# Performance work log

Hardware: AMD Instinct MI355X
Metric: run time of the kernel (lower is better)

Reference implementation:

```python
import jax, jax.numpy as jnp
import numpy as np

N_HEADS = 4
D_K = 64

def setup_inputs() -> dict:
    key = jax.random.key(0)
    k1, k2, k3 = jax.random.split(key, 3)
    B, C, H, W = 16, 256, 32, 32
    x = jax.random.normal(k1, (B, C, H, W), dtype=jnp.float32)
    # Linear(C, 3*n_heads*d_k) stored as [in, out] for x @ W
    w_proj = jax.random.normal(k2, (C, 3 * N_HEADS * D_K), dtype=jnp.float32) * (1.0 / np.sqrt(C))
    b_proj = jnp.zeros((3 * N_HEADS * D_K,), dtype=jnp.float32)
    w_out = jax.random.normal(k3, (N_HEADS * D_K, C), dtype=jnp.float32) * (1.0 / np.sqrt(N_HEADS * D_K))
    b_out = jnp.zeros((C,), dtype=jnp.float32)
    return {"x": x, "w_proj": w_proj, "b_proj": b_proj, "w_out": w_out, "b_out": b_out}

def reference(x, w_proj, b_proj, w_out, b_out):
    B, C, H, W = x.shape
    S = H * W
    scale = D_K ** -0.5
    xs = x.reshape(B, C, S).transpose(0, 2, 1)            # [B, S, C]
    qkv = (xs @ w_proj + b_proj).reshape(B, S, N_HEADS, 3 * D_K)
    q, k, v = jnp.split(qkv, 3, axis=3)                    # each [B, S, H, dk]
    attn = jnp.einsum('bihd,bjhd->bijh', q, k) * scale     # [B, S, S, heads]
    attn = jax.nn.softmax(attn, axis=2)
    o = jnp.einsum('bijh,bjhd->bihd', attn, v)             # [B, S, heads, dk]
    o = o.reshape(B, S, N_HEADS * D_K)
    res = o @ w_out + b_out + xs                           # [B, S, C]
    return res.transpose(0, 2, 1).reshape(B, C, H, W)
```

## Files before the change

### kernel.cpp

```cpp
#include <hip/hip_runtime.h>
#include <math.h>

#define B_  16
#define C_  256
#define S_  1024
#define NH  4
#define DK  64
#define P3  768
#define ND  256

typedef unsigned short u16;
typedef unsigned int   u32;
typedef float  f32x4  __attribute__((ext_vector_type(4)));
typedef short  bf16x8 __attribute__((ext_vector_type(8)));

#define MFMA16(a, b, c) __builtin_amdgcn_mfma_f32_16x16x32_bf16(a, b, c, 0, 0, 0)

#define QSCALE 0.1803368801111137f

__device__ __forceinline__ u16 f2bf(float f) {
    union { float f; u32 u; } x; x.f = f;
    u32 r = x.u + 0x7fffu + ((x.u >> 16) & 1u);
    return (u16)(r >> 16);
}

__device__ __forceinline__ void stage16(const u16* g, u16* l) {
    __builtin_amdgcn_global_load_lds(
        (const __attribute__((address_space(1))) void*)g,
        (__attribute__((address_space(3))) void*)l, 16, 0, 0);
}

__global__ __launch_bounds__(256) void transpose_cvt(
    const float* __restrict__ src, u16* __restrict__ dst, int R, int Cc)
{
    __shared__ float T[64][65];
    const int tid = threadIdx.x;
    const int c0 = blockIdx.x * 64, r0 = blockIdx.y * 64, z = blockIdx.z;
    src += (size_t)z * R * Cc;
    dst += (size_t)z * R * Cc;

    const int l64 = tid & 63, rr0 = tid >> 6;
    #pragma unroll
    for (int t = 0; t < 16; ++t) {
        int rr = rr0 + t * 4;
        T[rr][l64] = src[(size_t)(r0 + rr) * Cc + c0 + l64];
    }
    __syncthreads();
    const int rp = tid & 31;
    const int cb = tid >> 5;
    #pragma unroll
    for (int t = 0; t < 8; ++t) {
        int c = cb + t * 8;
        u32 lo = f2bf(T[2 * rp][c]);
        u32 hi = f2bf(T[2 * rp + 1][c]);
        *(u32*)&dst[(size_t)(c0 + c) * R + r0 + 2 * rp] = lo | (hi << 16);
    }
}

__global__ __launch_bounds__(256) void transpose_w(
    const float* __restrict__ wp, u16* __restrict__ wpT,
    const float* __restrict__ wo, u16* __restrict__ woT)
{
    const int z = blockIdx.z;
    const int Cc = z ? 256 : 768;
    if ((int)blockIdx.x * 64 >= Cc) return;
    const float* src = z ? wo : wp;
    u16* dst = z ? woT : wpT;
    const int R = 256;

    __shared__ float T[64][65];
    const int tid = threadIdx.x;
    const int c0 = blockIdx.x * 64, r0 = blockIdx.y * 64;

    const int l64 = tid & 63, rr0 = tid >> 6;
    #pragma unroll
    for (int t = 0; t < 16; ++t) {
        int rr = rr0 + t * 4;
        T[rr][l64] = src[(size_t)(r0 + rr) * Cc + c0 + l64];
    }
    __syncthreads();
    const int rp = tid & 31;
    const int cb = tid >> 5;
    #pragma unroll
    for (int t = 0; t < 8; ++t) {
        int c = cb + t * 8;
        u32 lo = f2bf(T[2 * rp][c]);
        u32 hi = f2bf(T[2 * rp + 1][c]);
        *(u32*)&dst[(size_t)(c0 + c) * R + r0 + 2 * rp] = lo | (hi << 16);
    }
}

__global__ __launch_bounds__(256) void qkv_mfma(
    const u16* __restrict__ xt, const u16* __restrict__ wpT,
    const float* __restrict__ bp, u16* __restrict__ qo,
    u16* __restrict__ ko, u16* __restrict__ vo)
{
    __shared__ __align__(16) u16 SM[24576];
    u16* As = SM;
    u16* Bs = SM + 16384;

    const int tid = threadIdx.x;
    const int w = tid >> 6, lane = tid & 63;
    const int n_ = lane & 15, quad = lane >> 4;
    const int n0 = blockIdx.x * 64, s0 = blockIdx.y * 128, b = blockIdx.z;

    const u16* ar0 = xt + ((size_t)b * S_ + s0 + (2 * w + 0) * 16 + n_) * C_ + quad * 8;
    const u16* ar1 = xt + ((size_t)b * S_ + s0 + (2 * w + 1) * 16 + n_) * C_ + quad * 8;
    const u16* br  = wpT + (size_t)(n0 + w * 16 + n_) * C_ + quad * 8;

    f32x4 acc[2][4];
    #pragma unroll
    for (int am = 0; am < 2; ++am)
        #pragma unroll
        for (int nf = 0; nf < 4; ++nf)
            #pragma unroll
            for (int r = 0; r < 4; ++r) acc[am][nf][r] = 0.f;

    #pragma unroll
    for (int kb = 0; kb < 2; ++kb) {
        const int kcb = kb * 128;
        __syncthreads();
        #pragma unroll
        for (int kc = 0; kc < 4; ++kc) {
            stage16(ar0 + kcb + kc * 32, As + ((2 * w + 0) * 4 + kc) * 512);
            stage16(ar1 + kcb + kc * 32, As + ((2 * w + 1) * 4 + kc) * 512);
            stage16(br  + kcb + kc * 32, Bs + (w * 4 + kc) * 512);
        }
        __syncthreads();
        #pragma unroll
        for (int kc = 0; kc < 4; ++kc) {
            bf16x8 af0 = *(const bf16x8*)&As[((2 * w + 0) * 4 + kc) * 512 + lane * 8];
            bf16x8 af1 = *(const bf16x8*)&As[((2 * w + 1) * 4 + kc) * 512 + lane * 8];
            #pragma unroll
            for (int nf = 0; nf < 4; ++nf) {
                bf16x8 bf = *(const bf16x8*)&Bs[(nf * 4 + kc) * 512 + lane * 8];
                acc[0][nf] = MFMA16(af0, bf, acc[0][nf]);
                acc[1][nf] = MFMA16(af1, bf, acc[1][nf]);
            }
        }
    }

    const int hd = n0 / 192, rem = n0 % 192, which = rem / 64;
    const int bh = b * NH + hd;
    float bias[4];
    #pragma unroll
    for (int nf = 0; nf < 4; ++nf) bias[nf] = bp[n0 + nf * 16 + n_];
    const float sc = (which == 0) ? QSCALE : 1.f;

    __syncthreads();
    if (which < 2) {
        u16* Cs = SM;
        #pragma unroll
        for (int am = 0; am < 2; ++am) {
            int row0 = w * 32 + am * 16 + quad * 4;
            #pragma unroll
            for (int nf = 0; nf < 4; ++nf)
                #pragma unroll
                for (int r = 0; r < 4; ++r)
                    Cs[(row0 + r) * 72 + nf * 16 + n_] =
                        f2bf((acc[am][nf][r] + bias[nf]) * sc);
        }
        __syncthreads();
        u16* dst = (which == 0) ? qo : ko;
        #pragma unroll
        for (int t = 0; t < 4; ++t) {
            int ii = tid + t * 256;
            int row = ii >> 3, c8 = (ii & 7) * 8;
            *(bf16x8*)&dst[((size_t)bh * S_ + s0 + row) * DK + c8] =
                *(const bf16x8*)&Cs[row * 72 + c8];
        }
    } else {
        u16* Cs = SM;
        #pragma unroll
        for (int am = 0; am < 2; ++am) {
            int colb = w * 32 + am * 16 + quad * 4;
            #pragma unroll
            for (int nf = 0; nf < 4; ++nf)
                #pragma unroll
                for (int r = 0; r < 4; ++r)
                    Cs[(nf * 16 + n_) * 136 + colb + r] =
                        f2bf(acc[am][nf][r] + bias[nf]);
        }
        __syncthreads();
        #pragma unroll
        for (int t = 0; t < 4; ++t) {
            int ii = tid + t * 256;
            int row = ii >> 4, c8 = (ii & 15) * 8;
            *(bf16x8*)&vo[((size_t)bh * DK + row) * S_ + s0 + c8] =
                *(const bf16x8*)&Cs[row * 136 + c8];
        }
    }
}

__global__ __launch_bounds__(256) void attn_mfma(
    const u16* __restrict__ q, const u16* __restrict__ k,
    const u16* __restrict__ vt, u16* __restrict__ obf)
{
    __shared__ __align__(16) u16 SM[9216];
    u16* Ks = SM;
    u16* Vs = SM + 4096;

    const int tid = threadIdx.x;
    const int w = tid >> 6, lane = tid & 63;
    const int n_ = lane & 15, quad = lane >> 4;
    const int i0 = blockIdx.x * 128;
    const int hd = blockIdx.y, b = blockIdx.z;
    const int bh = b * NH + hd;

    bf16x8 qf[2][2];
    #pragma unroll
    for (int am = 0; am < 2; ++am) {
        const u16* qrow = q + ((size_t)bh * S_ + i0 + w * 32 + am * 16 + n_) * DK;
        qf[am][0] = *(const bf16x8*)&qrow[quad * 8];
        qf[am][1] = *(const bf16x8*)&qrow[32 + quad * 8];
    }

    const int kappa = 32 * (w & 1) + 8 * (n_ >> 2) + 4 * (w >> 1) + (n_ & 3);
    const u16* kbase = k  + ((size_t)bh * S_ + kappa) * DK + quad * 8;
    const u16* vbase = vt + ((size_t)bh * DK + w * 16 + n_) * S_ + quad * 8;

    float lsum[2] = {0.f, 0.f};
    f32x4 oacc[2][4];
    #pragma unroll
    for (int am = 0; am < 2; ++am)
        #pragma unroll
        for (int nd = 0; nd < 4; ++nd)
            #pragma unroll
            for (int r = 0; r < 4; ++r) oacc[am][nd][r] = 0.f;

    for (int jt = 0; jt < S_; jt += 64) {
        __syncthreads();
        stage16(kbase + (size_t)jt * DK,      Ks + w * 1024);
        stage16(kbase + (size_t)jt * DK + 32, Ks + w * 1024 + 512);
        stage16(vbase + jt,                   Vs + w * 1024);
        stage16(vbase + jt + 32,              Vs + w * 1024 + 512);
        __syncthreads();

        f32x4 sb[2][4];
        #pragma unroll
        for (int nb = 0; nb < 4; ++nb) {
            bf16x8 kf0 = *(const bf16x8*)&Ks[nb * 1024 + lane * 8];
            bf16x8 kf1 = *(const bf16x8*)&Ks[nb * 1024 + 512 + lane * 8];
            #pragma unroll
            for (int am = 0; am < 2; ++am) {
                f32x4 a; a[0] = a[1] = a[2] = a[3] = 0.f;
                a = MFMA16(kf0, qf[am][0], a);
                a = MFMA16(kf1, qf[am][1], a);
                sb[am][nb] = a;
            }
        }

        bf16x8 pa[2][2];
        #pragma unroll
        for (int am = 0; am < 2; ++am) {
            u32 tr[4][4];
            #pragma unroll
            for (int nb = 0; nb < 4; ++nb)
                #pragma unroll
                for (int r = 0; r < 4; ++r) {
                    float p = exp2f(sb[am][nb][r]);
                    u32 bits = __float_as_uint(p) & 0xffff0000u;
                    lsum[am] += __uint_as_float(bits);
                    tr[nb][r] = bits;
                }
            union { bf16x8 v; u32 u[4]; } p0, p1;
            p0.u[0] = (tr[0][0] >> 16) | tr[0][1];
            p0.u[1] = (tr[0][2] >> 16) | tr[0][3];
            p0.u[2] = (tr[2][0] >> 16) | tr[2][1];
            p0.u[3] = (tr[2][2] >> 16) | tr[2][3];
            p1.u[0] = (tr[1][0] >> 16) | tr[1][1];
            p1.u[1] = (tr[1][2] >> 16) | tr[1][3];
            p1.u[2] = (tr[3][0] >> 16) | tr[3][1];
            p1.u[3] = (tr[3][2] >> 16) | tr[3][3];
            pa[am][0] = p0.v;
            pa[am][1] = p1.v;
        }

        #pragma unroll
        for (int nd = 0; nd < 4; ++nd) {
            bf16x8 vf0 = *(const bf16x8*)&Vs[nd * 1024 + lane * 8];
            bf16x8 vf1 = *(const bf16x8*)&Vs[nd * 1024 + 512 + lane * 8];
            #pragma unroll
            for (int am = 0; am < 2; ++am) {
                oacc[am][nd] = MFMA16(vf0, pa[am][0], oacc[am][nd]);
                oacc[am][nd] = MFMA16(vf1, pa[am][1], oacc[am][nd]);
            }
        }
    }

    float inv[2];
    #pragma unroll
    for (int am = 0; am < 2; ++am) {
        float s = lsum[am];
        s += __shfl_xor(s, 16);
        s += __shfl_xor(s, 32);
        inv[am] = 1.f / s;
    }

    __syncthreads();
    u16* eb = SM + w * 2304;
    #pragma unroll
    for (int am = 0; am < 2; ++am)
        #pragma unroll
        for (int nd = 0; nd < 4; ++nd) {
            uint2 uv;
            uv.x = (u32)f2bf(oacc[am][nd][0] * inv[am]) |
                   ((u32)f2bf(oacc[am][nd][1] * inv[am]) << 16);
            uv.y = (u32)f2bf(oacc[am][nd][2] * inv[am]) |
                   ((u32)f2bf(oacc[am][nd][3] * inv[am]) << 16);
            *(uint2*)&eb[(am * 16 + n_) * 72 + nd * 16 + quad * 4] = uv;
        }
    __syncthreads();
    #pragma unroll
    for (int t = 0; t < 4; ++t) {
        int ii = lane + t * 64;
        int row = ii >> 3, c8 = (ii & 7) * 8;
        *(bf16x8*)&obf[((size_t)b * S_ + i0 + w * 32 + row) * ND + hd * DK + c8] =
            *(const bf16x8*)&eb[row * 72 + c8];
    }
}

__global__ __launch_bounds__(256) void out_proj_mfma(
    const u16* __restrict__ obf, const u16* __restrict__ woT,
    const float* __restrict__ bo, const float* __restrict__ x,
    float* __restrict__ out)
{
    __shared__ __align__(16) u16 SM[24576];
    u16* Bs = SM;
    u16* As = SM + 16384;

    const int tid = threadIdx.x;
    const int w = tid >> 6, lane = tid & 63;
    const int n_ = lane & 15, quad = lane >> 4;
    const int c0 = blockIdx.x * 64, s0 = blockIdx.y * 128, b = blockIdx.z;

    const u16* ar  = woT + (size_t)(c0 + w * 16 + n_) * ND + quad * 8;
    const u16* br0 = obf + ((size_t)b * S_ + s0 + (2 * w + 0) * 16 + n_) * ND + quad * 8;
    const u16* br1 = obf + ((size_t)b * S_ + s0 + (2 * w + 1) * 16 + n_) * ND + quad * 8;

    f32x4 acc[2][4];
    #pragma unroll
    for (int nf = 0; nf < 2; ++nf)
        #pragma unroll
        for (int mb = 0; mb < 4; ++mb)
            #pragma unroll
            for (int r = 0; r < 4; ++r) acc[nf][mb][r] = 0.f;

    #pragma unroll
    for (int kb = 0; kb < 2; ++kb) {
        const int kcb = kb * 128;
        __syncthreads();
        #pragma unroll
        for (int kc = 0; kc < 4; ++kc) {
            stage16(ar  + kcb + kc * 32, As + (w * 4 + kc) * 512);
            stage16(br0 + kcb + kc * 32, Bs + ((2 * w + 0) * 4 + kc) * 512);
            stage16(br1 + kcb + kc * 32, Bs + ((2 * w + 1) * 4 + kc) * 512);
        }
        __syncthreads();
        #pragma unroll
        for (int kc = 0; kc < 4; ++kc) {
            bf16x8 bf0 = *(const bf16x8*)&Bs[((2 * w + 0) * 4 + kc) * 512 + lane * 8];
            bf16x8 bf1 = *(const bf16x8*)&Bs[((2 * w + 1) * 4 + kc) * 512 + lane * 8];
            #pragma unroll
            for (int mb = 0; mb < 4; ++mb) {
                bf16x8 af = *(const bf16x8*)&As[(mb * 4 + kc) * 512 + lane * 8];
                acc[0][mb] = MFMA16(af, bf0, acc[0][mb]);
                acc[1][mb] = MFMA16(af, bf1, acc[1][mb]);
            }
        }
    }

    #pragma unroll
    for (int mb = 0; mb < 4; ++mb)
        #pragma unroll
        for (int r = 0; r < 4; ++r) {
            int c = c0 + mb * 16 + quad * 4 + r;
            float bias = bo[c];
            #pragma unroll
            for (int nf = 0; nf < 2; ++nf) {
                size_t idx = ((size_t)b * C_ + c) * S_ + s0 + w * 32 + nf * 16 + n_;
                out[idx] = acc[nf][mb][r] + bias + x[idx];
            }
        }
}

extern "C" void kernel_launch(void* const* d_in, const int* in_sizes, int n_in,
                              void* d_out, int out_size, void* d_ws, size_t ws_size,
                              hipStream_t stream) {
    const float* x  = (const float*)d_in[0];
    const float* wp = (const float*)d_in[1];
    const float* bp = (const float*)d_in[2];
    const float* wo = (const float*)d_in[3];
    const float* bo = (const float*)d_in[4];
    float* out = (float*)d_out;

    const size_t QKV_E = (size_t)B_ * NH * S_ * DK;
    u16* q   = (u16*)d_ws;
    u16* kk  = q   + QKV_E;
    u16* vtp = kk  + QKV_E;
    u16* obf = vtp + QKV_E;
    u16* xt  = obf + (size_t)B_ * S_ * ND;
    u16* wpT = xt  + (size_t)B_ * S_ * C_;
    u16* woT = wpT + (size_t)P3 * C_;

    transpose_cvt<<<dim3(S_ / 64, C_ / 64, B_), 256, 0, stream>>>(x, xt, C_, S_);
    transpose_w  <<<dim3(12, 4, 2),             256, 0, stream>>>(wp, wpT, wo, woT);
    qkv_mfma     <<<dim3(P3 / 64, S_ / 128, B_), 256, 0, stream>>>(xt, wpT, bp, q, kk, vtp);
    attn_mfma    <<<dim3(S_ / 128, NH, B_),      256, 0, stream>>>(q, kk, vtp, obf);
    out_proj_mfma<<<dim3(C_ / 64, S_ / 128, B_), 256, 0, stream>>>(obf, woT, bo, x, out);
}
```

Measured before the change: 148.2 us.

## Double-buffer LDS staging in GEMM and attention kernels, merge transpose launches

The qkv, out-projection and attention kernels now use two LDS buffers. The next K-chunk or KV tile is issued with global_load_lds while the current one is computed, and manual vmcnt waits plus barriers replace the old sync-load-sync pattern. Attention MFMA sections also raise wave priority with s_setprio. The two transpose/convert kernels are merged into one launch to save launch overhead. LDS use per block grows in attention (doubled), which may reduce occupancy, and the manual waitcnt counts must match the number of outstanding loads for correctness.

Result: faster. 139.8 us (-5.7%).

```diff
diff --git a/kernel.cpp b/kernel.cpp
--- a/kernel.cpp
+++ b/kernel.cpp
@@ -18,6 +18,9 @@
 
 #define QSCALE 0.1803368801111137f
 
+#define WAITVM(N) asm volatile("s_waitcnt vmcnt(" #N ")" ::: "memory")
+#define BARRIER() asm volatile("s_barrier" ::: "memory")
+
 __device__ __forceinline__ u16 f2bf(float f) {
     union { float f; u32 u; } x; x.f = f;
     u32 r = x.u + 0x7fffu + ((x.u >> 16) & 1u);
@@ -30,43 +33,20 @@
         (__attribute__((address_space(3))) void*)l, 16, 0, 0);
 }
 
-__global__ __launch_bounds__(256) void transpose_cvt(
-    const float* __restrict__ src, u16* __restrict__ dst, int R, int Cc)
-{
-    __shared__ float T[64][65];
-    const int tid = threadIdx.x;
-    const int c0 = blockIdx.x * 64, r0 = blockIdx.y * 64, z = blockIdx.z;
-    src += (size_t)z * R * Cc;
-    dst += (size_t)z * R * Cc;
-
-    const int l64 = tid & 63, rr0 = tid >> 6;
-    #pragma unroll
-    for (int t = 0; t < 16; ++t) {
-        int rr = rr0 + t * 4;
-        T[rr][l64] = src[(size_t)(r0 + rr) * Cc + c0 + l64];
-    }
-    __syncthreads();
-    const int rp = tid & 31;
-    const int cb = tid >> 5;
-    #pragma unroll
-    for (int t = 0; t < 8; ++t) {
-        int c = cb + t * 8;
-        u32 lo = f2bf(T[2 * rp][c]);
-        u32 hi = f2bf(T[2 * rp + 1][c]);
-        *(u32*)&dst[(size_t)(c0 + c) * R + r0 + 2 * rp] = lo | (hi << 16);
-    }
-}
-
-__global__ __launch_bounds__(256) void transpose_w(
+__global__ __launch_bounds__(256) void transpose_all(
+    const float* __restrict__ x, u16* __restrict__ xt,
     const float* __restrict__ wp, u16* __restrict__ wpT,
     const float* __restrict__ wo, u16* __restrict__ woT)
 {
     const int z = blockIdx.z;
-    const int Cc = z ? 256 : 768;
+    const float* src;
+    u16* dst;
+    int Cc;
+    if (z < 16)       { src = x + (size_t)z * C_ * S_; dst = xt + (size_t)z * C_ * S_; Cc = S_; }
+    else if (z == 16) { src = wp; dst = wpT; Cc = P3; }
+    else              { src = wo; dst = woT; Cc = ND; }
     if ((int)blockIdx.x * 64 >= Cc) return;
-    const float* src = z ? wo : wp;
-    u16* dst = z ? woT : wpT;
-    const int R = 256;
+    const int R = C_;
 
     __shared__ float T[64][65];
     const int tid = threadIdx.x;
@@ -96,8 +76,6 @@
     u16* __restrict__ ko, u16* __restrict__ vo)
 {
     __shared__ __align__(16) u16 SM[24576];
-    u16* As = SM;
-    u16* Bs = SM + 16384;
 
     const int tid = threadIdx.x;
     const int w = tid >> 6, lane = tid & 63;
@@ -116,28 +94,48 @@
             #pragma unroll
             for (int r = 0; r < 4; ++r) acc[am][nf][r] = 0.f;
 
-    #pragma unroll
-    for (int kb = 0; kb < 2; ++kb) {
-        const int kcb = kb * 128;
-        __syncthreads();
-        #pragma unroll
-        for (int kc = 0; kc < 4; ++kc) {
-            stage16(ar0 + kcb + kc * 32, As + ((2 * w + 0) * 4 + kc) * 512);
-            stage16(ar1 + kcb + kc * 32, As + ((2 * w + 1) * 4 + kc) * 512);
-            stage16(br  + kcb + kc * 32, Bs + (w * 4 + kc) * 512);
-        }
-        __syncthreads();
-        #pragma unroll
-        for (int kc = 0; kc < 4; ++kc) {
-            bf16x8 af0 = *(const bf16x8*)&As[((2 * w + 0) * 4 + kc) * 512 + lane * 8];
-            bf16x8 af1 = *(const bf16x8*)&As[((2 * w + 1) * 4 + kc) * 512 + lane * 8];
+    {
+        u16* As_ = SM;
+        u16* Bs_ = SM + 8192;
+        stage16(ar0,      As_ + (4 * w + 0) * 512);
+        stage16(ar0 + 32, As_ + (4 * w + 1) * 512);
+        stage16(ar1,      As_ + (4 * w + 2) * 512);
+        stage16(ar1 + 32, As_ + (4 * w + 3) * 512);
+        stage16(br,       Bs_ + (2 * w + 0) * 512);
+        stage16(br + 32,  Bs_ + (2 * w + 1) * 512);
+    }
+
+    #pragma unroll
+    for (int p = 0; p < 4; ++p) {
+        u16* As_ = SM + (p & 1) * 12288;
+        u16* Bs_ = As_ + 8192;
+        if (p < 3) {
+            const int pk = (p + 1) * 64;
+            u16* An = SM + ((p + 1) & 1) * 12288;
+            u16* Bn = An + 8192;
+            stage16(ar0 + pk,      An + (4 * w + 0) * 512);
+            stage16(ar0 + pk + 32, An + (4 * w + 1) * 512);
+            stage16(ar1 + pk,      An + (4 * w + 2) * 512);
+            stage16(ar1 + pk + 32, An + (4 * w + 3) * 512);
+            stage16(br  + pk,      Bn + (2 * w + 0) * 512);
+            stage16(br  + pk + 32, Bn + (2 * w + 1) * 512);
+            WAITVM(6);
+        } else {
+            WAITVM(0);
+        }
+        BARRIER();
+        #pragma unroll
+        for (int kc = 0; kc < 2; ++kc) {
+            bf16x8 af0 = *(const bf16x8*)&As_[((2 * w + 0) * 2 + kc) * 512 + lane * 8];
+            bf16x8 af1 = *(const bf16x8*)&As_[((2 * w + 1) * 2 + kc) * 512 + lane * 8];
             #pragma unroll
             for (int nf = 0; nf < 4; ++nf) {
-                bf16x8 bf = *(const bf16x8*)&Bs[(nf * 4 + kc) * 512 + lane * 8];
+                bf16x8 bf = *(const bf16x8*)&Bs_[(nf * 2 + kc) * 512 + lane * 8];
                 acc[0][nf] = MFMA16(af0, bf, acc[0][nf]);
                 acc[1][nf] = MFMA16(af1, bf, acc[1][nf]);
             }
         }
+        if (p < 3) BARRIER();
     }
 
     const int hd = n0 / 192, rem = n0 % 192, which = rem / 64;
@@ -196,9 +194,7 @@
     const u16* __restrict__ q, const u16* __restrict__ k,
     const u16* __restrict__ vt, u16* __restrict__ obf)
 {
-    __shared__ __align__(16) u16 SM[9216];
-    u16* Ks = SM;
-    u16* Vs = SM + 4096;
+    __shared__ __align__(16) u16 SM[16384];
 
     const int tid = threadIdx.x;
     const int w = tid >> 6, lane = tid & 63;
@@ -228,15 +224,30 @@
             #pragma unroll
             for (int r = 0; r < 4; ++r) oacc[am][nd][r] = 0.f;
 
-    for (int jt = 0; jt < S_; jt += 64) {
-        __syncthreads();
-        stage16(kbase + (size_t)jt * DK,      Ks + w * 1024);
-        stage16(kbase + (size_t)jt * DK + 32, Ks + w * 1024 + 512);
-        stage16(vbase + jt,                   Vs + w * 1024);
-        stage16(vbase + jt + 32,              Vs + w * 1024 + 512);
-        __syncthreads();
+    stage16(kbase,      SM + w * 1024);
+    stage16(kbase + 32, SM + w * 1024 + 512);
+    stage16(vbase,      SM + 4096 + w * 1024);
+    stage16(vbase + 32, SM + 4096 + w * 1024 + 512);
+
+    for (int t = 0; t < 16; ++t) {
+        u16* Ks = SM + (t & 1) * 8192;
+        u16* Vs = Ks + 4096;
+        if (t < 15) {
+            const size_t jn = (size_t)(t + 1) * 64;
+            u16* Kn = SM + ((t + 1) & 1) * 8192;
+            u16* Vn = Kn + 4096;
+            stage16(kbase + jn * DK,      Kn + w * 1024);
+            stage16(kbase + jn * DK + 32, Kn + w * 1024 + 512);
+            stage16(vbase + jn,           Vn + w * 1024);
+            stage16(vbase + jn + 32,      Vn + w * 1024 + 512);
+            WAITVM(4);
+        } else {
+            WAITVM(0);
+        }
+        BARRIER();
 
         f32x4 sb[2][4];
+        __builtin_amdgcn_s_setprio(1);
         #pragma unroll
         for (int nb = 0; nb < 4; ++nb) {
             bf16x8 kf0 = *(const bf16x8*)&Ks[nb * 1024 + lane * 8];
@@ -249,6 +260,7 @@
                 sb[am][nb] = a;
             }
         }
+        __builtin_amdgcn_s_setprio(0);
 
         bf16x8 pa[2][2];
         #pragma unroll
@@ -276,6 +288,7 @@
             pa[am][1] = p1.v;
         }
 
+        __builtin_amdgcn_s_setprio(1);
         #pragma unroll
         for (int nd = 0; nd < 4; ++nd) {
             bf16x8 vf0 = *(const bf16x8*)&Vs[nd * 1024 + lane * 8];
@@ -286,6 +299,9 @@
                 oacc[am][nd] = MFMA16(vf1, pa[am][1], oacc[am][nd]);
             }
         }
+        __builtin_amdgcn_s_setprio(0);
+
+        if (t < 15) BARRIER();
     }
 
     float inv[2];
@@ -326,8 +342,6 @@
     float* __restrict__ out)
 {
     __shared__ __align__(16) u16 SM[24576];
-    u16* Bs = SM;
-    u16* As = SM + 16384;
 
     const int tid = threadIdx.x;
     const int w = tid >> 6, lane = tid & 63;
@@ -346,28 +360,48 @@
             #pragma unroll
             for (int r = 0; r < 4; ++r) acc[nf][mb][r] = 0.f;
 
-    #pragma unroll
-    for (int kb = 0; kb < 2; ++kb) {
-        const int kcb = kb * 128;
-        __syncthreads();
-        #pragma unroll
-        for (int kc = 0; kc < 4; ++kc) {
-            stage16(ar  + kcb + kc * 32, As + (w * 4 + kc) * 512);
-            stage16(br0 + kcb + kc * 32, Bs + ((2 * w + 0) * 4 + kc) * 512);
-            stage16(br1 + kcb + kc * 32, Bs + ((2 * w + 1) * 4 + kc) * 512);
-        }
-        __syncthreads();
-        #pragma unroll
-        for (int kc = 0; kc < 4; ++kc) {
-            bf16x8 bf0 = *(const bf16x8*)&Bs[((2 * w + 0) * 4 + kc) * 512 + lane * 8];
-            bf16x8 bf1 = *(const bf16x8*)&Bs[((2 * w + 1) * 4 + kc) * 512 + lane * 8];
+    {
+        u16* Bs_ = SM;
+        u16* As_ = SM + 8192;
+        stage16(br0,      Bs_ + (4 * w + 0) * 512);
+        stage16(br0 + 32, Bs_ + (4 * w + 1) * 512);
+        stage16(br1,      Bs_ + (4 * w + 2) * 512);
+        stage16(br1 + 32, Bs_ + (4 * w + 3) * 512);
+        stage16(ar,       As_ + (2 * w + 0) * 512);
+        stage16(ar + 32,  As_ + (2 * w + 1) * 512);
+    }
+
+    #pragma unroll
+    for (int p = 0; p < 4; ++p) {
+        u16* Bs_ = SM + (p & 1) * 12288;
+        u16* As_ = Bs_ + 8192;
+        if (p < 3) {
+            const int pk = (p + 1) * 64;
+            u16* Bn = SM + ((p + 1) & 1) * 12288;
+            u16* An = Bn + 8192;
+            stage16(br0 + pk,      Bn + (4 * w + 0) * 512);
+            stage16(br0 + pk + 32, Bn + (4 * w + 1) * 512);
+            stage16(br1 + pk,      Bn + (4 * w + 2) * 512);
+            stage16(br1 + pk + 32, Bn + (4 * w + 3) * 512);
+            stage16(ar  + pk,      An + (2 * w + 0) * 512);
+            stage16(ar  + pk + 32, An + (2 * w + 1) * 512);
+            WAITVM(6);
+        } else {
+            WAITVM(0);
+        }
+        BARRIER();
+        #pragma unroll
+        for (int kc = 0; kc < 2; ++kc) {
+            bf16x8 bf0 = *(const bf16x8*)&Bs_[((2 * w + 0) * 2 + kc) * 512 + lane * 8];
+            bf16x8 bf1 = *(const bf16x8*)&Bs_[((2 * w + 1) * 2 + kc) * 512 + lane * 8];
             #pragma unroll
             for (int mb = 0; mb < 4; ++mb) {
-                bf16x8 af = *(const bf16x8*)&As[(mb * 4 + kc) * 512 + lane * 8];
+                bf16x8 af = *(const bf16x8*)&As_[(mb * 2 + kc) * 512 + lane * 8];
                 acc[0][mb] = MFMA16(af, bf0, acc[0][mb]);
                 acc[1][mb] = MFMA16(af, bf1, acc[1][mb]);
             }
         }
+        if (p < 3) BARRIER();
     }
 
     #pragma unroll
@@ -403,8 +437,7 @@
     u16* wpT = xt  + (size_t)B_ * S_ * C_;
     u16* woT = wpT + (size_t)P3 * C_;
 
-    transpose_cvt<<<dim3(S_ / 64, C_ / 64, B_), 256, 0, stream>>>(x, xt, C_, S_);
-    transpose_w  <<<dim3(12, 4, 2),             256, 0, stream>>>(wp, wpT, wo, woT);
+    transpose_all<<<dim3(16, 4, 18),             256, 0, stream>>>(x, xt, wp, wpT, wo, woT);
     qkv_mfma     <<<dim3(P3 / 64, S_ / 128, B_), 256, 0, stream>>>(xt, wpT, bp, q, kk, vtp);
     attn_mfma    <<<dim3(S_ / 128, NH, B_),      256, 0, stream>>>(q, kk, vtp, obf);
     out_proj_mfma<<<dim3(C_ / 64, S_ / 128, B_), 256, 0, stream>>>(obf, woT, bo, x, out);
```
